# Optimization experiments

Hardware: AMD Instinct MI355X
Metric: run time of the kernel (lower is better)

## Reference

```python
import jax, jax.numpy as jnp
import numpy as np

C_Z = 128
C_HIDDEN = 128
N_RES = 384
B = 1
EPS = 1e-5


def _layernorm(x, w, b):
    mu = jnp.mean(x, axis=-1, keepdims=True)
    var = jnp.mean(jnp.square(x - mu), axis=-1, keepdims=True)
    return (x - mu) * jax.lax.rsqrt(var + EPS) * w + b


def setup_inputs() -> dict:
    key = jax.random.key(0)
    ks = jax.random.split(key, 16)
    s_z = 1.0 / np.sqrt(C_Z)
    s_h = 1.0 / np.sqrt(C_HIDDEN)
    return {
        "z": jax.random.normal(ks[0], (B, N_RES, N_RES, C_Z), dtype=jnp.float32),
        "mask": jnp.ones((B, N_RES, N_RES), dtype=jnp.float32),
        "ln_in_w": jnp.ones((C_Z,), jnp.float32),
        "ln_in_b": jnp.zeros((C_Z,), jnp.float32),
        "a_g_w": jax.random.normal(ks[1], (C_HIDDEN, C_Z), jnp.float32) * s_z,
        "a_g_b": jnp.zeros((C_HIDDEN,), jnp.float32),
        "a_p_w": jax.random.normal(ks[2], (C_HIDDEN, C_Z), jnp.float32) * s_z,
        "a_p_b": jnp.zeros((C_HIDDEN,), jnp.float32),
        "b_g_w": jax.random.normal(ks[3], (C_HIDDEN, C_Z), jnp.float32) * s_z,
        "b_g_b": jnp.zeros((C_HIDDEN,), jnp.float32),
        "b_p_w": jax.random.normal(ks[4], (C_HIDDEN, C_Z), jnp.float32) * s_z,
        "b_p_b": jnp.zeros((C_HIDDEN,), jnp.float32),
        "g_w": jax.random.normal(ks[5], (C_Z, C_Z), jnp.float32) * s_z,
        "g_b": jnp.zeros((C_Z,), jnp.float32),
        "ln_out_w": jnp.ones((C_HIDDEN,), jnp.float32),
        "ln_out_b": jnp.zeros((C_HIDDEN,), jnp.float32),
        "z_w": jax.random.normal(ks[6], (C_Z, C_HIDDEN), jnp.float32) * s_h,
        "z_b": jnp.zeros((C_Z,), jnp.float32),
    }


def reference(z, mask, ln_in_w, ln_in_b, a_g_w, a_g_b, a_p_w, a_p_b,
              b_g_w, b_g_b, b_p_w, b_p_b, g_w, g_b,
              ln_out_w, ln_out_b, z_w, z_b):
    # z: [B, N, N, c_z]; mask: [B, N, N]
    m = mask[..., None]
    zn = _layernorm(z, ln_in_w, ln_in_b)
    # gated projections (fused LN+GEMM+sigmoid*mul in the Triton kernel)
    a = m * jax.nn.sigmoid(jnp.einsum("bijc,hc->bijh", zn, a_g_w) + a_g_b) \
          * (jnp.einsum("bijc,hc->bijh", zn, a_p_w) + a_p_b)
    b = m * jax.nn.sigmoid(jnp.einsum("bijc,hc->bijh", zn, b_g_w) + b_g_b) \
          * (jnp.einsum("bijc,hc->bijh", zn, b_p_w) + b_p_b)
    # outgoing triangle update: contract over third node k, per channel
    x = jnp.einsum("bikh,bjkh->bijh", a, b)
    # output path: sigmoid(gate(zn)) * linear_z(LN_out(x))
    xn = _layernorm(x, ln_out_w, ln_out_b)
    gate = jax.nn.sigmoid(jnp.einsum("bijc,oc->bijo", zn, g_w) + g_b)
    out = gate * (jnp.einsum("bijh,oh->bijo", xn, z_w) + z_b)
    return out
```

## Files before the change

kernel.cpp:

```cpp
#include <hip/hip_runtime.h>

#define NRES 384
#define CD   128
#define MTOT (NRES*NRES)

typedef unsigned short u16;
typedef __bf16 bf16x8 __attribute__((ext_vector_type(8)));
typedef float  f32x16 __attribute__((ext_vector_type(16)));

static __device__ __forceinline__ u16 f2bf(float f) {
  __bf16 b = (__bf16)f;
  return __builtin_bit_cast(u16, b);
}
static __device__ __forceinline__ float bf2f(u16 v) {
  return __uint_as_float(((unsigned)v) << 16);
}
static __device__ __forceinline__ float sigmoidf(float x) {
  return 1.0f / (1.0f + __expf(-x));
}

static __device__ __forceinline__ void gl16(const void* g, void* l) {
  __builtin_amdgcn_global_load_lds(
      (const __attribute__((address_space(1))) void*)g,
      (__attribute__((address_space(3))) void*)l, 16, 0, 0);
}

__global__ void k_cvt_w(const float* w0, const float* w1, const float* w2,
                        const float* w3, const float* w4, const float* w5,
                        u16* wb) {
  int i = blockIdx.x * 256 + threadIdx.x;
  const float* srcs[6] = {w0, w1, w2, w3, w4, w5};
  wb[i] = f2bf(srcs[i >> 14][i & 16383]);
}

__global__ __launch_bounds__(256) void k_ln_in(const float* __restrict__ z,
                                               const float* __restrict__ w,
                                               const float* __restrict__ b,
                                               u16* __restrict__ zn) {
  int wv = threadIdx.x >> 6, lane = threadIdx.x & 63;
  float2 wv2 = ((const float2*)w)[lane];
  float2 bv2 = ((const float2*)b)[lane];
  for (int rr = 0; rr < 4; ++rr) {
    size_t row = (size_t)blockIdx.x * 16 + wv * 4 + rr;
    float2 v = ((const float2*)(z + row * CD))[lane];
    float s = v.x + v.y;
#pragma unroll
    for (int off = 32; off >= 1; off >>= 1) s += __shfl_xor(s, off);
    float mu = s * (1.0f / CD);
    float dx = v.x - mu, dy = v.y - mu;
    float vr = dx * dx + dy * dy;
#pragma unroll
    for (int off = 32; off >= 1; off >>= 1) vr += __shfl_xor(vr, off);
    float rs = rsqrtf(vr * (1.0f / CD) + 1e-5f);
    ushort2 o;
    o.x = f2bf(dx * rs * wv2.x + bv2.x);
    o.y = f2bf(dy * rs * wv2.y + bv2.y);
    ((ushort2*)(zn + row * CD))[lane] = o;
  }
}

__global__ __launch_bounds__(256) void k_proj(
    const u16* __restrict__ zn, const float* __restrict__ mask,
    const u16* __restrict__ wb,
    const float* __restrict__ agb, const float* __restrict__ apb,
    const float* __restrict__ bgb, const float* __restrict__ bpb,
    u16* __restrict__ a_out, u16* __restrict__ b_out) {
  int type = blockIdx.y;
  int m_base = blockIdx.x * 256;
  int lane = threadIdx.x & 63;
  int wvu = __builtin_amdgcn_readfirstlane(threadIdx.x >> 6);
  int nl = lane & 31, s = lane >> 5;
  int h = wvu * 32 + nl;

  const u16* wgp = (type == 0) ? wb : wb + 32768;
  const u16* wpp = (type == 0) ? wb + 16384 : wb + 49152;
  const float* bgp = (type == 0) ? agb : bgb;
  const float* bpp = (type == 0) ? apb : bpb;
  u16* outp = (type == 0) ? a_out : b_out;

  __shared__ u16 znt[2][64][128];

  bf16x8 wgf[8], wpf[8];
#pragma unroll
  for (int kk = 0; kk < 8; ++kk) {
    wgf[kk] = *(const bf16x8*)(wgp + h * CD + kk * 16 + s * 8);
    wpf[kk] = *(const bf16x8*)(wpp + h * CD + kk * 16 + s * 8);
  }

  int rl = lane >> 4, p16 = lane & 15;
#define STAGE_ZNT(mt, bf)                                                   \
  {                                                                         \
    _Pragma("unroll")                                                       \
    for (int j = 0; j < 4; ++j) {                                           \
      int row = wvu * 16 + j * 4 + rl;                                      \
      int gc = (p16 ^ (row & 7)) << 3;                                      \
      gl16(zn + (size_t)((mt) + row) * CD + gc, &znt[bf][wvu * 16 + j * 4][0]); \
    }                                                                       \
  }

  STAGE_ZNT(m_base, 0);
  __syncthreads();

  for (int ms = 0; ms < 4; ++ms) {
    int cur = ms & 1;
    if (ms < 3) STAGE_ZNT(m_base + (ms + 1) * 64, cur ^ 1);
    int mt = m_base + ms * 64;

    f32x16 accg[2], accp[2];
#pragma unroll
    for (int i = 0; i < 16; ++i) { accg[0][i] = 0; accg[1][i] = 0; accp[0][i] = 0; accp[1][i] = 0; }
#pragma unroll
    for (int kk = 0; kk < 8; ++kk) {
      int c = ((kk * 2 + s) ^ (nl & 7)) << 3;
      bf16x8 zf0 = *(const bf16x8*)&znt[cur][nl][c];
      bf16x8 zf1 = *(const bf16x8*)&znt[cur][32 + nl][c];
      accg[0] = __builtin_amdgcn_mfma_f32_32x32x16_bf16(wgf[kk], zf0, accg[0], 0, 0, 0);
      accg[1] = __builtin_amdgcn_mfma_f32_32x32x16_bf16(wgf[kk], zf1, accg[1], 0, 0, 0);
      accp[0] = __builtin_amdgcn_mfma_f32_32x32x16_bf16(wpf[kk], zf0, accp[0], 0, 0, 0);
      accp[1] = __builtin_amdgcn_mfma_f32_32x32x16_bf16(wpf[kk], zf1, accp[1], 0, 0, 0);
    }
    __syncthreads();
    float mk0 = mask[mt + nl];
    float mk1 = mask[mt + 32 + nl];
#pragma unroll
    for (int r = 0; r < 16; ++r) {
      int hh = wvu * 32 + (r & 3) + 8 * (r >> 2) + 4 * s;
      float bg = bgp[hh], bp = bpp[hh];
      u16* rowp = outp + (size_t)hh * MTOT + mt + nl;
      rowp[0]  = f2bf(mk0 * sigmoidf(accg[0][r] + bg) * (accp[0][r] + bp));
      rowp[32] = f2bf(mk1 * sigmoidf(accg[1][r] + bg) * (accp[1][r] + bp));
    }
  }
#undef STAGE_ZNT
}

__global__ __launch_bounds__(256) void k_tri(const u16* __restrict__ a,
                                             const u16* __restrict__ b,
                                             u16* __restrict__ x) {
  int h  = blockIdx.y;
  int tm = blockIdx.x / 3, tn = blockIdx.x % 3;
  int i0 = tm * 128, j0 = tn * 128;
  const u16* ah = a + (size_t)h * MTOT;
  const u16* bh = b + (size_t)h * MTOT;

  __shared__ u16 At[2][128][64];
  __shared__ u16 Bt[2][128][64];

  int lane = threadIdx.x & 63;
  int wvu = __builtin_amdgcn_readfirstlane(threadIdx.x >> 6);
  int nl = lane & 31, s = lane >> 5;
  int wr = wvu >> 1, wc = wvu & 1;
  int rl = lane >> 3, p8 = lane & 7;

  f32x16 acc[4];
#pragma unroll
  for (int q = 0; q < 4; ++q)
#pragma unroll
    for (int i = 0; i < 16; ++i) acc[q][i] = 0;

#define STAGE_TRI(bf, k0)                                                     \
  {                                                                           \
    _Pragma("unroll")                                                         \
    for (int j = 0; j < 4; ++j) {                                             \
      int row = wvu * 32 + j * 8 + rl;                                        \
      int gc = (p8 ^ (rl & 7)) << 3;                                          \
      gl16(ah + (size_t)(i0 + row) * NRES + (k0) + gc, &At[bf][wvu * 32 + j * 8][0]); \
      gl16(bh + (size_t)(j0 + row) * NRES + (k0) + gc, &Bt[bf][wvu * 32 + j * 8][0]); \
    }                                                                         \
  }

  STAGE_TRI(0, 0);
  __syncthreads();

  for (int kb = 0; kb < 6; ++kb) {
    int cur = kb & 1;
    if (kb < 5) STAGE_TRI(cur ^ 1, (kb + 1) * 64);
#pragma unroll
    for (int kk = 0; kk < 4; ++kk) {
      int c = ((kk * 2 + s) ^ (nl & 7)) << 3;
      bf16x8 af0 = *(const bf16x8*)&At[cur][wr * 64 + nl][c];
      bf16x8 af1 = *(const bf16x8*)&At[cur][wr * 64 + 32 + nl][c];
      bf16x8 bf0 = *(const bf16x8*)&Bt[cur][wc * 64 + nl][c];
      bf16x8 bf1 = *(const bf16x8*)&Bt[cur][wc * 64 + 32 + nl][c];
      acc[0] = __builtin_amdgcn_mfma_f32_32x32x16_bf16(af0, bf0, acc[0], 0, 0, 0);
      acc[1] = __builtin_amdgcn_mfma_f32_32x32x16_bf16(af0, bf1, acc[1], 0, 0, 0);
      acc[2] = __builtin_amdgcn_mfma_f32_32x32x16_bf16(af1, bf0, acc[2], 0, 0, 0);
      acc[3] = __builtin_amdgcn_mfma_f32_32x32x16_bf16(af1, bf1, acc[3], 0, 0, 0);
    }
    __syncthreads();
  }
#undef STAGE_TRI

  u16* xh = x + (size_t)h * MTOT;
#pragma unroll
  for (int msub = 0; msub < 2; ++msub)
#pragma unroll
    for (int nsub = 0; nsub < 2; ++nsub) {
      int j = j0 + wc * 64 + nsub * 32 + nl;
#pragma unroll
      for (int r = 0; r < 16; ++r) {
        int i = i0 + wr * 64 + msub * 32 + (r & 3) + 8 * (r >> 2) + 4 * s;
        xh[(size_t)i * NRES + j] = f2bf(acc[msub * 2 + nsub][r]);
      }
    }
}

__global__ __launch_bounds__(256) void k_out(
    const u16* __restrict__ x, const u16* __restrict__ zn,
    const u16* __restrict__ wb, const float* __restrict__ gb,
    const float* __restrict__ lnw, const float* __restrict__ lnb,
    const float* __restrict__ zb, float* __restrict__ out) {
  int m0 = blockIdx.x * 64;
  int t = threadIdx.x;
  int wv = t >> 6, lane = t & 63, nl = lane & 31, s = lane >> 5;
  int o = wv * 32 + nl;

  __shared__ u16 tile[64][136];

  const u16* gwp = wb + 4 * 16384;
  const u16* zwp = wb + 5 * 16384;

  bf16x8 gwf[8];
#pragma unroll
  for (int kk = 0; kk < 8; ++kk)
    gwf[kk] = *(const bf16x8*)(gwp + o * CD + kk * 16 + s * 8);

#pragma unroll
  for (int it = 0; it < 4; ++it) {
    int idx = it * 256 + t;
    int r = idx >> 4, c8 = idx & 15;
    *(uint4*)&tile[r][c8 * 8] =
        *(const uint4*)(zn + (size_t)(m0 + r) * CD + c8 * 8);
  }
  __syncthreads();

  f32x16 gacc[2];
#pragma unroll
  for (int i = 0; i < 16; ++i) { gacc[0][i] = 0; gacc[1][i] = 0; }
#pragma unroll
  for (int kk = 0; kk < 8; ++kk) {
    bf16x8 zf0 = *(const bf16x8*)&tile[nl][kk * 16 + s * 8];
    bf16x8 zf1 = *(const bf16x8*)&tile[32 + nl][kk * 16 + s * 8];
    gacc[0] = __builtin_amdgcn_mfma_f32_32x32x16_bf16(zf0, gwf[kk], gacc[0], 0, 0, 0);
    gacc[1] = __builtin_amdgcn_mfma_f32_32x32x16_bf16(zf1, gwf[kk], gacc[1], 0, 0, 0);
  }
  float gbv = gb[o];
  float gv[32];
#pragma unroll
  for (int ms = 0; ms < 2; ++ms)
#pragma unroll
    for (int r = 0; r < 16; ++r)
      gv[ms * 16 + r] = sigmoidf(gacc[ms][r] + gbv);
  __syncthreads();

  bf16x8 zwf[8];
#pragma unroll
  for (int kk = 0; kk < 8; ++kk)
    zwf[kk] = *(const bf16x8*)(zwp + o * CD + kk * 16 + s * 8);

#pragma unroll
  for (int ps = 0; ps < 2; ++ps) {
    int idx = ps * 256 + t;
    int hp = idx >> 3, mc = idx & 7;
    uint4 v0 = *(const uint4*)(x + (size_t)(2 * hp)     * MTOT + m0 + mc * 8);
    uint4 v1 = *(const uint4*)(x + (size_t)(2 * hp + 1) * MTOT + m0 + mc * 8);
    unsigned c0[4] = {v0.x, v0.y, v0.z, v0.w};
    unsigned c1[4] = {v1.x, v1.y, v1.z, v1.w};
#pragma unroll
    for (int q = 0; q < 4; ++q) {
      ushort2 lo, hi;
      lo.x = (u16)(c0[q] & 0xffffu); lo.y = (u16)(c1[q] & 0xffffu);
      hi.x = (u16)(c0[q] >> 16);     hi.y = (u16)(c1[q] >> 16);
      *(ushort2*)&tile[mc * 8 + 2 * q][2 * hp]     = lo;
      *(ushort2*)&tile[mc * 8 + 2 * q + 1][2 * hp] = hi;
    }
  }
  __syncthreads();

  int r = t >> 2, q = t & 3;
  float vals[32];
  float sum = 0;
#pragma unroll
  for (int j = 0; j < 32; ++j) { float v = bf2f(tile[r][q * 32 + j]); vals[j] = v; sum += v; }
  sum += __shfl_xor(sum, 1);
  sum += __shfl_xor(sum, 2);
  float mu = sum * (1.0f / CD);
  float var = 0;
#pragma unroll
  for (int j = 0; j < 32; ++j) { float d = vals[j] - mu; var += d * d; }
  var += __shfl_xor(var, 1);
  var += __shfl_xor(var, 2);
  float rs = rsqrtf(var * (1.0f / CD) + 1e-5f);
#pragma unroll
  for (int j = 0; j < 32; ++j) {
    int hh = q * 32 + j;
    tile[r][hh] = f2bf((vals[j] - mu) * rs * lnw[hh] + lnb[hh]);
  }
  __syncthreads();

  f32x16 acc[2];
#pragma unroll
  for (int i = 0; i < 16; ++i) { acc[0][i] = 0; acc[1][i] = 0; }
#pragma unroll
  for (int kk = 0; kk < 8; ++kk) {
    bf16x8 af0 = *(const bf16x8*)&tile[nl][kk * 16 + s * 8];
    bf16x8 af1 = *(const bf16x8*)&tile[32 + nl][kk * 16 + s * 8];
    acc[0] = __builtin_amdgcn_mfma_f32_32x32x16_bf16(af0, zwf[kk], acc[0], 0, 0, 0);
    acc[1] = __builtin_amdgcn_mfma_f32_32x32x16_bf16(af1, zwf[kk], acc[1], 0, 0, 0);
  }

  float zbv = zb[o];
#pragma unroll
  for (int ms = 0; ms < 2; ++ms)
#pragma unroll
    for (int rr = 0; rr < 16; ++rr) {
      int rowoff = (rr & 3) + 8 * (rr >> 2) + 4 * s;
      int mg = m0 + ms * 32 + rowoff;
      out[(size_t)mg * CD + o] = gv[ms * 16 + rr] * (acc[ms][rr] + zbv);
    }
}

extern "C" void kernel_launch(void* const* d_in, const int* in_sizes, int n_in,
                              void* d_out, int out_size, void* d_ws, size_t ws_size,
                              hipStream_t stream) {
  const float* z       = (const float*)d_in[0];
  const float* mask    = (const float*)d_in[1];
  const float* ln_in_w = (const float*)d_in[2];
  const float* ln_in_b = (const float*)d_in[3];
  const float* a_g_w   = (const float*)d_in[4];
  const float* a_g_b   = (const float*)d_in[5];
  const float* a_p_w   = (const float*)d_in[6];
  const float* a_p_b   = (const float*)d_in[7];
  const float* b_g_w   = (const float*)d_in[8];
  const float* b_g_b   = (const float*)d_in[9];
  const float* b_p_w   = (const float*)d_in[10];
  const float* b_p_b   = (const float*)d_in[11];
  const float* g_w     = (const float*)d_in[12];
  const float* g_b     = (const float*)d_in[13];
  const float* ln_o_w  = (const float*)d_in[14];
  const float* ln_o_b  = (const float*)d_in[15];
  const float* z_w     = (const float*)d_in[16];
  const float* z_b     = (const float*)d_in[17];
  float* out = (float*)d_out;

  const size_t SZ = (size_t)MTOT * CD * sizeof(u16);
  char* w = (char*)d_ws;
  u16* zn = (u16*)(w);
  u16* a  = (u16*)(w + SZ);
  u16* b  = (u16*)(w + 2 * SZ);
  u16* x  = (u16*)(w + 3 * SZ);
  u16* wb = (u16*)(w + 4 * SZ);
  (void)ws_size; (void)in_sizes; (void)n_in; (void)out_size;

  k_cvt_w<<<384, 256, 0, stream>>>(a_g_w, a_p_w, b_g_w, b_p_w, g_w, z_w, wb);
  k_ln_in<<<MTOT / 16, 256, 0, stream>>>(z, ln_in_w, ln_in_b, zn);
  k_proj<<<dim3(MTOT / 256, 2), 256, 0, stream>>>(zn, mask, wb,
      a_g_b, a_p_b, b_g_b, b_p_b, a, b);
  k_tri<<<dim3(9, 128), 256, 0, stream>>>(a, b, x);
  k_out<<<MTOT / 64, 256, 0, stream>>>(x, zn, wb, g_b, ln_o_w, ln_o_b, z_b, out);
}
```

Before: 299.9 us.

## Fuse a/b projections in one block sharing a fully staged zn tile

```diff
diff --git a/kernel.cpp b/kernel.cpp
--- a/kernel.cpp
+++ b/kernel.cpp
@@ -16,7 +16,7 @@
   return __uint_as_float(((unsigned)v) << 16);
 }
 static __device__ __forceinline__ float sigmoidf(float x) {
-  return 1.0f / (1.0f + __expf(-x));
+  return __builtin_amdgcn_rcpf(1.0f + __expf(-x));
 }
 
 static __device__ __forceinline__ void gl16(const void* g, void* l) {
@@ -65,73 +65,85 @@
     const float* __restrict__ agb, const float* __restrict__ apb,
     const float* __restrict__ bgb, const float* __restrict__ bpb,
     u16* __restrict__ a_out, u16* __restrict__ b_out) {
-  int type = blockIdx.y;
   int m_base = blockIdx.x * 256;
   int lane = threadIdx.x & 63;
   int wvu = __builtin_amdgcn_readfirstlane(threadIdx.x >> 6);
   int nl = lane & 31, s = lane >> 5;
   int h = wvu * 32 + nl;
 
-  const u16* wgp = (type == 0) ? wb : wb + 32768;
-  const u16* wpp = (type == 0) ? wb + 16384 : wb + 49152;
-  const float* bgp = (type == 0) ? agb : bgb;
-  const float* bpp = (type == 0) ? apb : bpb;
-  u16* outp = (type == 0) ? a_out : b_out;
-
-  __shared__ u16 znt[2][64][128];
-
-  bf16x8 wgf[8], wpf[8];
-#pragma unroll
-  for (int kk = 0; kk < 8; ++kk) {
-    wgf[kk] = *(const bf16x8*)(wgp + h * CD + kk * 16 + s * 8);
-    wpf[kk] = *(const bf16x8*)(wpp + h * CD + kk * 16 + s * 8);
-  }
+  __shared__ u16 znt[256][128];
 
   int rl = lane >> 4, p16 = lane & 15;
-#define STAGE_ZNT(mt, bf)                                                   \
-  {                                                                         \
-    _Pragma("unroll")                                                       \
-    for (int j = 0; j < 4; ++j) {                                           \
-      int row = wvu * 16 + j * 4 + rl;                                      \
-      int gc = (p16 ^ (row & 7)) << 3;                                      \
-      gl16(zn + (size_t)((mt) + row) * CD + gc, &znt[bf][wvu * 16 + j * 4][0]); \
-    }                                                                       \
-  }
-
-  STAGE_ZNT(m_base, 0);
-  __syncthreads();
-
+#pragma unroll
+  for (int j = 0; j < 16; ++j) {
+    int row = wvu * 64 + j * 4 + rl;
+    int gc = (p16 ^ (row & 7)) << 3;
+    gl16(zn + (size_t)(m_base + row) * CD + gc, &znt[wvu * 64 + j * 4][0]);
+  }
+
+  float mk0[4], mk1[4];
+#pragma unroll
   for (int ms = 0; ms < 4; ++ms) {
-    int cur = ms & 1;
-    if (ms < 3) STAGE_ZNT(m_base + (ms + 1) * 64, cur ^ 1);
-    int mt = m_base + ms * 64;
-
-    f32x16 accg[2], accp[2];
-#pragma unroll
-    for (int i = 0; i < 16; ++i) { accg[0][i] = 0; accg[1][i] = 0; accp[0][i] = 0; accp[1][i] = 0; }
+    mk0[ms] = mask[m_base + ms * 64 + nl];
+    mk1[ms] = mask[m_base + ms * 64 + 32 + nl];
+  }
+  __syncthreads();
+
+#pragma unroll 1
+  for (int type = 0; type < 2; ++type) {
+    const u16* wgp = wb + type * 32768;
+    const u16* wpp = wgp + 16384;
+    const float* bgp = (type == 0) ? agb : bgb;
+    const float* bpp = (type == 0) ? apb : bpb;
+    u16* outp = (type == 0) ? a_out : b_out;
+
+    bf16x8 wgf[8], wpf[8];
 #pragma unroll
     for (int kk = 0; kk < 8; ++kk) {
-      int c = ((kk * 2 + s) ^ (nl & 7)) << 3;
-      bf16x8 zf0 = *(const bf16x8*)&znt[cur][nl][c];
-      bf16x8 zf1 = *(const bf16x8*)&znt[cur][32 + nl][c];
-      accg[0] = __builtin_amdgcn_mfma_f32_32x32x16_bf16(wgf[kk], zf0, accg[0], 0, 0, 0);
-      accg[1] = __builtin_amdgcn_mfma_f32_32x32x16_bf16(wgf[kk], zf1, accg[1], 0, 0, 0);
-      accp[0] = __builtin_amdgcn_mfma_f32_32x32x16_bf16(wpf[kk], zf0, accp[0], 0, 0, 0);
-      accp[1] = __builtin_amdgcn_mfma_f32_32x32x16_bf16(wpf[kk], zf1, accp[1], 0, 0, 0);
-    }
-    __syncthreads();
-    float mk0 = mask[mt + nl];
-    float mk1 = mask[mt + 32 + nl];
-#pragma unroll
-    for (int r = 0; r < 16; ++r) {
-      int hh = wvu * 32 + (r & 3) + 8 * (r >> 2) + 4 * s;
-      float bg = bgp[hh], bp = bpp[hh];
-      u16* rowp = outp + (size_t)hh * MTOT + mt + nl;
-      rowp[0]  = f2bf(mk0 * sigmoidf(accg[0][r] + bg) * (accp[0][r] + bp));
-      rowp[32] = f2bf(mk1 * sigmoidf(accg[1][r] + bg) * (accp[1][r] + bp));
-    }
-  }
-#undef STAGE_ZNT
+      wgf[kk] = *(const bf16x8*)(wgp + h * CD + kk * 16 + s * 8);
+      wpf[kk] = *(const bf16x8*)(wpp + h * CD + kk * 16 + s * 8);
+    }
+    float4 bg4[4], bp4[4];
+#pragma unroll
+    for (int q = 0; q < 4; ++q) {
+      bg4[q] = *(const float4*)(bgp + wvu * 32 + 4 * s + 8 * q);
+      bp4[q] = *(const float4*)(bpp + wvu * 32 + 4 * s + 8 * q);
+    }
+
+#pragma unroll 1
+    for (int ms = 0; ms < 4; ++ms) {
+      int mt = m_base + ms * 64;
+      f32x16 accg[2], accp[2];
+#pragma unroll
+      for (int i = 0; i < 16; ++i) {
+        accg[0][i] = 0; accg[1][i] = 0; accp[0][i] = 0; accp[1][i] = 0;
+      }
+#pragma unroll
+      for (int kk = 0; kk < 8; ++kk) {
+        int c = ((kk * 2 + s) ^ (nl & 7)) << 3;
+        bf16x8 zf0 = *(const bf16x8*)&znt[ms * 64 + nl][c];
+        bf16x8 zf1 = *(const bf16x8*)&znt[ms * 64 + 32 + nl][c];
+        accg[0] = __builtin_amdgcn_mfma_f32_32x32x16_bf16(wgf[kk], zf0, accg[0], 0, 0, 0);
+        accg[1] = __builtin_amdgcn_mfma_f32_32x32x16_bf16(wgf[kk], zf1, accg[1], 0, 0, 0);
+        accp[0] = __builtin_amdgcn_mfma_f32_32x32x16_bf16(wpf[kk], zf0, accp[0], 0, 0, 0);
+        accp[1] = __builtin_amdgcn_mfma_f32_32x32x16_bf16(wpf[kk], zf1, accp[1], 0, 0, 0);
+      }
+#pragma unroll
+      for (int r = 0; r < 16; ++r) {
+        int hh = wvu * 32 + (r & 3) + 8 * (r >> 2) + 4 * s;
+        float bg, bp;
+        switch (r >> 2) {
+          case 0: bg = ((const float*)&bg4[0])[r & 3]; bp = ((const float*)&bp4[0])[r & 3]; break;
+          case 1: bg = ((const float*)&bg4[1])[r & 3]; bp = ((const float*)&bp4[1])[r & 3]; break;
+          case 2: bg = ((const float*)&bg4[2])[r & 3]; bp = ((const float*)&bp4[2])[r & 3]; break;
+          default: bg = ((const float*)&bg4[3])[r & 3]; bp = ((const float*)&bp4[3])[r & 3]; break;
+        }
+        u16* rowp = outp + (size_t)hh * MTOT + mt + nl;
+        rowp[0]  = f2bf(mk0[ms] * sigmoidf(accg[0][r] + bg) * (accp[0][r] + bp));
+        rowp[32] = f2bf(mk1[ms] * sigmoidf(accg[1][r] + bg) * (accp[1][r] + bp));
+      }
+    }
+  }
 }
 
 __global__ __launch_bounds__(256) void k_tri(const u16* __restrict__ a,
@@ -354,7 +366,7 @@
 
   k_cvt_w<<<384, 256, 0, stream>>>(a_g_w, a_p_w, b_g_w, b_p_w, g_w, z_w, wb);
   k_ln_in<<<MTOT / 16, 256, 0, stream>>>(z, ln_in_w, ln_in_b, zn);
-  k_proj<<<dim3(MTOT / 256, 2), 256, 0, stream>>>(zn, mask, wb,
+  k_proj<<<MTOT / 256, 256, 0, stream>>>(zn, mask, wb,
       a_g_b, a_p_b, b_g_b, b_p_b, a, b);
   k_tri<<<dim3(9, 128), 256, 0, stream>>>(a, b, x);
   k_out<<<MTOT / 64, 256, 0, stream>>>(x, zn, wb, g_b, ln_o_w, ln_o_b, z_b, out);
```

Measured after the change: 294.7 us. Within noise of the previous version (-1.7%).

## Triple-buffer projection kernel staging with explicit waitcnt and single barrier

Applied to the files above, without the earlier changes.

```diff
diff --git a/kernel.cpp b/kernel.cpp
--- a/kernel.cpp
+++ b/kernel.cpp
@@ -16,7 +16,7 @@
   return __uint_as_float(((unsigned)v) << 16);
 }
 static __device__ __forceinline__ float sigmoidf(float x) {
-  return 1.0f / (1.0f + __expf(-x));
+  return __builtin_amdgcn_rcpf(1.0f + __expf(-x));
 }
 
 static __device__ __forceinline__ void gl16(const void* g, void* l) {
@@ -29,8 +29,10 @@
                         const float* w3, const float* w4, const float* w5,
                         u16* wb) {
   int i = blockIdx.x * 256 + threadIdx.x;
-  const float* srcs[6] = {w0, w1, w2, w3, w4, w5};
-  wb[i] = f2bf(srcs[i >> 14][i & 16383]);
+  int which = blockIdx.x >> 6;
+  const float* src = (which == 0) ? w0 : (which == 1) ? w1 : (which == 2) ? w2
+                   : (which == 3) ? w3 : (which == 4) ? w4 : w5;
+  wb[i] = f2bf(src[i & 16383]);
 }
 
 __global__ __launch_bounds__(256) void k_ln_in(const float* __restrict__ z,
@@ -67,18 +69,30 @@
     u16* __restrict__ a_out, u16* __restrict__ b_out) {
   int type = blockIdx.y;
   int m_base = blockIdx.x * 256;
-  int lane = threadIdx.x & 63;
-  int wvu = __builtin_amdgcn_readfirstlane(threadIdx.x >> 6);
+  int t = threadIdx.x;
+  int lane = t & 63;
+  int wvu = __builtin_amdgcn_readfirstlane(t >> 6);
   int nl = lane & 31, s = lane >> 5;
   int h = wvu * 32 + nl;
 
-  const u16* wgp = (type == 0) ? wb : wb + 32768;
-  const u16* wpp = (type == 0) ? wb + 16384 : wb + 49152;
+  const u16* wgp = wb + (size_t)type * 32768;
+  const u16* wpp = wgp + 16384;
   const float* bgp = (type == 0) ? agb : bgb;
   const float* bpp = (type == 0) ? apb : bpb;
   u16* outp = (type == 0) ? a_out : b_out;
 
-  __shared__ u16 znt[2][64][128];
+  __shared__ u16 znt[3][64][128];
+  __shared__ float bsl[2][128];
+
+  if (t < 128) bsl[0][t] = bgp[t];
+  else         bsl[1][t - 128] = bpp[t - 128];
+
+  float mk0[4], mk1[4];
+#pragma unroll
+  for (int ms = 0; ms < 4; ++ms) {
+    mk0[ms] = mask[m_base + ms * 64 + nl];
+    mk1[ms] = mask[m_base + ms * 64 + 32 + nl];
+  }
 
   bf16x8 wgf[8], wpf[8];
 #pragma unroll
@@ -98,39 +112,53 @@
     }                                                                       \
   }
 
+  asm volatile("" ::: "memory");
   STAGE_ZNT(m_base, 0);
-  __syncthreads();
-
-  for (int ms = 0; ms < 4; ++ms) {
-    int cur = ms & 1;
-    if (ms < 3) STAGE_ZNT(m_base + (ms + 1) * 64, cur ^ 1);
-    int mt = m_base + ms * 64;
-
-    f32x16 accg[2], accp[2];
-#pragma unroll
-    for (int i = 0; i < 16; ++i) { accg[0][i] = 0; accg[1][i] = 0; accp[0][i] = 0; accp[1][i] = 0; }
-#pragma unroll
-    for (int kk = 0; kk < 8; ++kk) {
-      int c = ((kk * 2 + s) ^ (nl & 7)) << 3;
-      bf16x8 zf0 = *(const bf16x8*)&znt[cur][nl][c];
-      bf16x8 zf1 = *(const bf16x8*)&znt[cur][32 + nl][c];
-      accg[0] = __builtin_amdgcn_mfma_f32_32x32x16_bf16(wgf[kk], zf0, accg[0], 0, 0, 0);
-      accg[1] = __builtin_amdgcn_mfma_f32_32x32x16_bf16(wgf[kk], zf1, accg[1], 0, 0, 0);
-      accp[0] = __builtin_amdgcn_mfma_f32_32x32x16_bf16(wpf[kk], zf0, accp[0], 0, 0, 0);
-      accp[1] = __builtin_amdgcn_mfma_f32_32x32x16_bf16(wpf[kk], zf1, accp[1], 0, 0, 0);
-    }
-    __syncthreads();
-    float mk0 = mask[mt + nl];
-    float mk1 = mask[mt + 32 + nl];
-#pragma unroll
-    for (int r = 0; r < 16; ++r) {
-      int hh = wvu * 32 + (r & 3) + 8 * (r >> 2) + 4 * s;
-      float bg = bgp[hh], bp = bpp[hh];
-      u16* rowp = outp + (size_t)hh * MTOT + mt + nl;
-      rowp[0]  = f2bf(mk0 * sigmoidf(accg[0][r] + bg) * (accp[0][r] + bp));
-      rowp[32] = f2bf(mk1 * sigmoidf(accg[1][r] + bg) * (accp[1][r] + bp));
-    }
-  }
+  asm volatile("" ::: "memory");
+  STAGE_ZNT(m_base + 64, 1);
+  asm volatile("" ::: "memory");
+
+  asm volatile("s_waitcnt lgkmcnt(0)" ::: "memory");
+
+#define PROJ_ITER(ms, buf, WAITINSN, STAGEIT, stbuf)                          \
+  {                                                                           \
+    asm volatile(WAITINSN ::: "memory");                                      \
+    __builtin_amdgcn_s_barrier();                                             \
+    asm volatile("" ::: "memory");                                            \
+    f32x16 accg0, accg1, accp0, accp1;                                        \
+    _Pragma("unroll")                                                         \
+    for (int i = 0; i < 16; ++i) {                                            \
+      accg0[i] = 0; accg1[i] = 0; accp0[i] = 0; accp1[i] = 0;                 \
+    }                                                                         \
+    _Pragma("unroll")                                                         \
+    for (int kk = 0; kk < 8; ++kk) {                                          \
+      int c = ((kk * 2 + s) ^ (nl & 7)) << 3;                                 \
+      bf16x8 zf0 = *(const bf16x8*)&znt[buf][nl][c];                          \
+      bf16x8 zf1 = *(const bf16x8*)&znt[buf][32 + nl][c];                     \
+      accg0 = __builtin_amdgcn_mfma_f32_32x32x16_bf16(wgf[kk], zf0, accg0, 0, 0, 0); \
+      accg1 = __builtin_amdgcn_mfma_f32_32x32x16_bf16(wgf[kk], zf1, accg1, 0, 0, 0); \
+      accp0 = __builtin_amdgcn_mfma_f32_32x32x16_bf16(wpf[kk], zf0, accp0, 0, 0, 0); \
+      accp1 = __builtin_amdgcn_mfma_f32_32x32x16_bf16(wpf[kk], zf1, accp1, 0, 0, 0); \
+    }                                                                         \
+    int mt = m_base + (ms) * 64;                                              \
+    _Pragma("unroll")                                                         \
+    for (int r = 0; r < 16; ++r) {                                            \
+      int hh = wvu * 32 + (r & 3) + 8 * (r >> 2) + 4 * s;                     \
+      float bg = bsl[0][hh], bp = bsl[1][hh];                                 \
+      u16* rowp = outp + (size_t)hh * MTOT + mt + nl;                         \
+      rowp[0]  = f2bf(mk0[ms] * sigmoidf(accg0[r] + bg) * (accp0[r] + bp));   \
+      rowp[32] = f2bf(mk1[ms] * sigmoidf(accg1[r] + bg) * (accp1[r] + bp));   \
+    }                                                                         \
+    asm volatile("" ::: "memory");                                            \
+    if (STAGEIT) STAGE_ZNT(m_base + ((ms) + 2) * 64, stbuf);                  \
+    asm volatile("" ::: "memory");                                            \
+  }
+
+  PROJ_ITER(0, 0, "s_waitcnt vmcnt(4)", 1, 2);
+  PROJ_ITER(1, 1, "s_waitcnt vmcnt(4)", 1, 0);
+  PROJ_ITER(2, 2, "s_waitcnt vmcnt(4)", 0, 0);
+  PROJ_ITER(3, 0, "s_waitcnt vmcnt(0)", 0, 0);
+#undef PROJ_ITER
 #undef STAGE_ZNT
 }
 
```

After: 284.9 us. 5.0% less time.
